# Optimization experiments

Hardware: AMD Instinct MI355X
Metric: run time of the kernel (lower is better)

## Reference

```python
import jax, jax.numpy as jnp
import numpy as np

B, G, S, C = 64, 2048, 64, 3


def setup_inputs() -> dict:
    key = jax.random.key(0)
    k1, k2 = jax.random.split(key)
    neighbor = jax.random.normal(k1, (B, G, S, C), dtype=jnp.float32)
    center = jax.random.normal(k2, (B, G, C), dtype=jnp.float32)
    return {"neighbor": neighbor, "center": center}


def _disambiguate_vector_directions(lps, vecs):
    # lps: [B,G,S,3] local points; vecs: [B,G,3] candidate axes.
    knn = lps.shape[2]
    proj = jnp.sum(vecs[:, :, None, :] * lps, axis=3)                 # [B,G,S]
    n_pos = jnp.sum((proj > 0).astype(jnp.float32), axis=2, keepdims=True)  # [B,G,1]
    flip = (n_pos < 0.5 * knn).astype(jnp.float32)
    return (1.0 - 2.0 * flip) * vecs


def reference(neighbor, center):
    # neighbor: [B,G,S,3] (C==3 path -> axis1/axis2 both PCA)
    pos = neighbor[..., 0:3]
    # Distance-based weights for weighted PCA covariance.
    norms = jnp.linalg.norm(pos, axis=3, keepdims=True)               # [B,G,S,1]
    max_norms = jnp.max(norms, axis=2, keepdims=True)                 # [B,G,1,1]
    w = max_norms - norms
    w = w / (jnp.sum(w, axis=2, keepdims=True) + 1e-6)
    scaled_pos = 100.0 * pos
    # Weighted covariance: [B,G,3,3]
    covs = jnp.einsum('bgsk,bgsl->bgkl', w * scaled_pos, scaled_pos)
    # Symmetric 3x3 eigendecomposition, eigenvalues ascending, eigenvectors as columns
    # (same convention as pytorch3d symeig3x3; signs fixed by disambiguation below).
    _, eigvec = jnp.linalg.eigh(covs)                                 # [B,G,3,3]
    z_axis = _disambiguate_vector_directions(pos, eigvec[:, :, :, 0])  # smallest-eig
    x_axis = _disambiguate_vector_directions(pos, eigvec[:, :, :, 2])  # largest-eig
    y_axis = jnp.cross(z_axis, x_axis)                                # [B,G,3]
    lrfs = jnp.stack((z_axis, y_axis, x_axis), axis=3)                # [B,G,3,3] (columns)
    # Rotate local points into the LRF: batched [S,3] x [3,3]
    rot_neighbor = jnp.einsum('bgsc,bgcd->bgsd', pos, lrfs)           # [B,G,S,3]
    return (rot_neighbor, lrfs)
```

## Files before the change

### kernel.cpp

```cpp
#include <hip/hip_runtime.h>
#include <math.h>


__device__ __forceinline__ float slapy2_(float x, float y) {
    _Pragma("clang fp contract(off)")
    float xa = fabsf(x), ya = fabsf(y);
    float w = fmaxf(xa, ya), z = fminf(xa, ya);
    if (z == 0.0f) return w;
    float t = z / w;
    return w * sqrtf(1.0f + t * t);
}

__device__ __forceinline__ void slartg_(float f, float g,
                                        float &c, float &s, float &r) {
    _Pragma("clang fp contract(off)")
    if (g == 0.0f) { c = 1.0f; s = 0.0f; r = f; return; }
    if (f == 0.0f) { c = 0.0f; s = (g >= 0.0f) ? 1.0f : -1.0f; r = fabsf(g); return; }
    float d = sqrtf(f * f + g * g);
    float p = 1.0f / d;
    c = fabsf(f) * p;
    s = g * ((f >= 0.0f) ? p : -p);
    r = (f >= 0.0f) ? d : -d;
}

__device__ __forceinline__ void slaev2_(float a, float b, float cc,
                                        float &rt1, float &rt2,
                                        float &cs1, float &sn1) {
    _Pragma("clang fp contract(off)")
    float sm = a + cc, df = a - cc;
    float adf = fabsf(df);
    float tb = b + b;
    float ab = fabsf(tb);
    float acmx, acmn;
    if (fabsf(a) > fabsf(cc)) { acmx = a; acmn = cc; } else { acmx = cc; acmn = a; }
    float rt;
    if (adf > ab)      { float t = ab / adf; rt = adf * sqrtf(1.0f + t * t); }
    else if (adf < ab) { float t = adf / ab; rt = ab * sqrtf(1.0f + t * t); }
    else                rt = ab * sqrtf(2.0f);
    int sgn1;
    if (sm < 0.0f)      { rt1 = 0.5f * (sm - rt); sgn1 = -1; rt2 = (acmx / rt1) * acmn - (b / rt1) * b; }
    else if (sm > 0.0f) { rt1 = 0.5f * (sm + rt); sgn1 =  1; rt2 = (acmx / rt1) * acmn - (b / rt1) * b; }
    else                { rt1 = 0.5f * rt; rt2 = -0.5f * rt; sgn1 = 1; }
    int sgn2;
    float cs;
    if (df >= 0.0f) { cs = df + rt; sgn2 = 1; } else { cs = df - rt; sgn2 = -1; }
    float acs = fabsf(cs);
    if (acs > ab) {
        float ct = -tb / cs;
        sn1 = 1.0f / sqrtf(1.0f + ct * ct);
        cs1 = ct * sn1;
    } else {
        if (ab == 0.0f) { cs1 = 1.0f; sn1 = 0.0f; }
        else {
            float tn = -cs / tb;
            cs1 = 1.0f / sqrtf(1.0f + tn * tn);
            sn1 = tn * cs1;
        }
    }
    if (sgn1 == sgn2) { float tn = cs1; cs1 = -sn1; sn1 = tn; }
}

__device__ __forceinline__ float getd3(int i, float d1, float d2, float d3) {
    return (i == 1) ? d1 : ((i == 2) ? d2 : d3);
}
__device__ __forceinline__ void setd3(int i, float v, float &d1, float &d2, float &d3) {
    d1 = (i == 1) ? v : d1;
    d2 = (i == 2) ? v : d2;
    d3 = (i == 3) ? v : d3;
}
__device__ __forceinline__ float gete2(int i, float e1, float e2) {
    return (i == 1) ? e1 : e2;
}
__device__ __forceinline__ void sete2(int i, float v, float &e1, float &e2) {
    e1 = (i == 1) ? v : e1;
    e2 = (i == 2) ? v : e2;
}

__device__ __forceinline__ void zrot3r(int j, float ctemp, float stemp,
                                       float &z11, float &z12, float &z13,
                                       float &z21, float &z22, float &z23,
                                       float &z31, float &z32, float &z33) {
    _Pragma("clang fp contract(off)")
    if (j == 1) {
        { float t = z12; z12 = (ctemp * t) - (stemp * z11); z11 = (stemp * t) + (ctemp * z11); }
        { float t = z22; z22 = (ctemp * t) - (stemp * z21); z21 = (stemp * t) + (ctemp * z21); }
        { float t = z32; z32 = (ctemp * t) - (stemp * z31); z31 = (stemp * t) + (ctemp * z31); }
    } else {
        { float t = z13; z13 = (ctemp * t) - (stemp * z12); z12 = (stemp * t) + (ctemp * z12); }
        { float t = z23; z23 = (ctemp * t) - (stemp * z22); z22 = (stemp * t) + (ctemp * z22); }
        { float t = z33; z33 = (ctemp * t) - (stemp * z32); z32 = (stemp * t) + (ctemp * z32); }
    }
}

__device__ __forceinline__ void ssteqr3_reg(
        float &d1_, float &d2_, float &d3_, float &e1_, float &e2_,
        float &z11, float &z12, float &z13,
        float &z21, float &z22, float &z23,
        float &z31, float &z32, float &z33) {
    _Pragma("clang fp contract(off)")
    const float EPS    = 5.9604644775390625e-8f;
    const float EPS2   = EPS * EPS;
    const float SAFMIN = 1.17549435e-38f;
    const int n = 3, nmaxit = 3 * 30;
    int jtot = 0, l1 = 1;

#define GD(i)      getd3((i), d1_, d2_, d3_)
#define SD(i, v)   setd3((i), (v), d1_, d2_, d3_)
#define GE(i)      gete2((i), e1_, e2_)
#define SE(i, v)   sete2((i), (v), e1_, e2_)
#define ZR(j, c, s) zrot3r((j), (c), (s), z11, z12, z13, z21, z22, z23, z31, z32, z33)

    while (true) {
        if (l1 > n) break;
        if (l1 > 1) SE(l1 - 1, 0.0f);
        int m = n;
        for (int mm = l1; mm <= n - 1; ++mm) {
            float tst = fabsf(GE(mm));
            if (tst == 0.0f) { m = mm; break; }
            if (tst <= (sqrtf(fabsf(GD(mm))) * sqrtf(fabsf(GD(mm + 1)))) * EPS) {
                SE(mm, 0.0f); m = mm; break;
            }
        }
        int l = l1, lsv = l, lend = m, lendsv = lend;
        l1 = m + 1;
        if (lend == l) continue;
        if (fabsf(GD(lend)) < fabsf(GD(l))) { lend = lsv; l = lendsv; }

        if (lend > l) {
            while (true) {
                m = lend;
                if (l != lend) {
                    for (int mm = l; mm <= lend - 1; ++mm) {
                        float em = GE(mm);
                        float tst = em * em;
                        if (tst <= (EPS2 * fabsf(GD(mm))) * fabsf(GD(mm + 1)) + SAFMIN) { m = mm; break; }
                    }
                }
                if (m < lend) SE(m, 0.0f);
                float p = GD(l);
                if (m == l) {
                    SD(l, p); ++l;
                    if (l <= lend) continue;
                    break;
                }
                if (m == l + 1) {
                    float rt1, rt2, c, s;
                    slaev2_(GD(l), GE(l), GD(l + 1), rt1, rt2, c, s);
                    ZR(l, c, s);
                    SD(l, rt1); SD(l + 1, rt2); SE(l, 0.0f);
                    l += 2;
                    if (l <= lend) continue;
                    break;
                }
                if (jtot == nmaxit) break;
                ++jtot;
                {
                    float el = GE(l);
                    float g = (GD(l + 1) - p) / (2.0f * el);
                    float r = slapy2_(g, 1.0f);
                    g = GD(m) - p + el / (g + ((g >= 0.0f) ? r : -r));
                    float s = 1.0f, c = 1.0f;
                    p = 0.0f;
                    for (int i = m - 1; i >= l; --i) {
                        float ei = GE(i);
                        float f = s * ei;
                        float b = c * ei;
                        slartg_(g, f, c, s, r);
                        if (i != m - 1) SE(i + 1, r);
                        g = GD(i + 1) - p;
                        float r2 = ((GD(i) - g) * s) + ((2.0f * c) * b);
                        p = s * r2;
                        SD(i + 1, g + p);
                        g = (c * r2) - b;
                        ZR(i, c, -s);
                    }
                    SD(l, GD(l) - p);
                    SE(l, g);
                }
            }
        } else if (lend < l) {
            while (true) {
                m = lend;
                if (l != lend) {
                    for (int mm = l; mm >= lend + 1; --mm) {
                        float em = GE(mm - 1);
                        float tst = em * em;
                        if (tst <= (EPS2 * fabsf(GD(mm))) * fabsf(GD(mm - 1)) + SAFMIN) { m = mm; break; }
                    }
                }
                if (m > lend) SE(m - 1, 0.0f);
                float p = GD(l);
                if (m == l) {
                    SD(l, p); --l;
                    if (l >= lend) continue;
                    break;
                }
                if (m == l - 1) {
                    float rt1, rt2, c, s;
                    slaev2_(GD(l - 1), GE(l - 1), GD(l), rt1, rt2, c, s);
                    ZR(l - 1, c, s);
                    SD(l - 1, rt1); SD(l, rt2); SE(l - 1, 0.0f);
                    l -= 2;
                    if (l >= lend) continue;
                    break;
                }
                if (jtot == nmaxit) break;
                ++jtot;
                {
                    float el = GE(l - 1);
                    float g = (GD(l - 1) - p) / (2.0f * el);
                    float r = slapy2_(g, 1.0f);
                    g = GD(m) - p + el / (g + ((g >= 0.0f) ? r : -r));
                    float s = 1.0f, c = 1.0f;
                    p = 0.0f;
                    for (int i = m; i <= l - 1; ++i) {
                        float ei = GE(i);
                        float f = s * ei;
                        float b = c * ei;
                        slartg_(g, f, c, s, r);
                        if (i != m) SE(i - 1, r);
                        g = GD(i) - p;
                        float r2 = ((GD(i + 1) - g) * s) + ((2.0f * c) * b);
                        p = s * r2;
                        SD(i, g + p);
                        g = (c * r2) - b;
                        ZR(i, c, s);
                    }
                    SD(l, GD(l) - p);
                    SE(l - 1, g);
                }
            }
        }
    }
    {
        int k = 1; float p = d1_;
        if (d2_ < p) { k = 2; p = d2_; }
        if (d3_ < p) { k = 3; p = d3_; }
        if (k == 2) {
            d2_ = d1_; d1_ = p;
            float t;
            t = z11; z11 = z12; z12 = t;
            t = z21; z21 = z22; z22 = t;
            t = z31; z31 = z32; z32 = t;
        } else if (k == 3) {
            d3_ = d1_; d1_ = p;
            float t;
            t = z11; z11 = z13; z13 = t;
            t = z21; z21 = z23; z23 = t;
            t = z31; z31 = z33; z33 = t;
        }
        if (d3_ < d2_) {
            float t = d2_; d2_ = d3_; d3_ = t;
            t = z12; z12 = z13; z13 = t;
            t = z22; z22 = z23; z23 = t;
            t = z32; z32 = z33; z33 = t;
        }
    }
#undef GD
#undef SD
#undef GE
#undef SE
#undef ZR
}

__device__ __forceinline__ float nrm3_(float x, float y, float z) {
    _Pragma("clang fp contract(off)")
    float t = (x * x) + (y * y);
    t = t + (z * z);
    return sqrtf(t);
}

__device__ __forceinline__ void covstep(float px, float py, float pz, float wq,
                                        float &c00, float &c10, float &c20,
                                        float &c11, float &c21, float &c22) {
    _Pragma("clang fp contract(off)")
    const float spx = 100.0f * px, spy = 100.0f * py, spz = 100.0f * pz;
    const float ax = wq * spx, ay = wq * spy, az = wq * spz;
    c00 = c00 + (ax * spx);
    c10 = c10 + (ay * spx);
    c20 = c20 + (az * spx);
    c11 = c11 + (ay * spy);
    c21 = c21 + (az * spy);
    c22 = c22 + (az * spz);
}

__device__ __forceinline__ void rotstep(float px, float py, float pz,
                                        float zv0, float zv1, float zv2,
                                        float yv0, float yv1, float yv2,
                                        float xv0, float xv1, float xv2,
                                        float &ra, float &rb, float &rc) {
    _Pragma("clang fp contract(off)")
    ra = ((px * zv0) + (py * zv1)) + (pz * zv2);
    rb = ((px * yv0) + (py * yv1)) + (pz * yv2);
    rc = ((px * xv0) + (py * xv1)) + (pz * xv2);
}

__global__ __launch_bounds__(256, 4) void lrf_kernel(const float* __restrict__ nbr,
                                                     float* __restrict__ rot,
                                                     float* __restrict__ lrf) {
    _Pragma("clang fp contract(off)")
    __shared__ float wql[64 * 65];
    const int tid = threadIdx.x;
    const int gl  = tid >> 2;
    const int k   = tid & 3;
    const int g   = (blockIdx.x << 6) + gl;
    const int lbase = gl * 65;

    const float4* __restrict__ p4 = reinterpret_cast<const float4*>(nbr)
                                    + (long long)g * 48 + k * 12;
    const float4* __restrict__ q4 = reinterpret_cast<const float4*>(nbr)
                                    + (long long)g * 48;

    float mx = -3.402823466e+38f;
#pragma unroll
    for (int q = 0; q < 4; ++q) {
        const float4 v0 = p4[q * 3 + 0];
        const float4 v1 = p4[q * 3 + 1];
        const float4 v2 = p4[q * 3 + 2];
        const float n0 = nrm3_(v0.x, v0.y, v0.z);
        const float n1 = nrm3_(v0.w, v1.x, v1.y);
        const float n2 = nrm3_(v1.z, v1.w, v2.x);
        const float n3 = nrm3_(v2.y, v2.z, v2.w);
        const int b = lbase + 16 * k + 4 * q;
        wql[b + 0] = n0;
        wql[b + 1] = n1;
        wql[b + 2] = n2;
        wql[b + 3] = n3;
        mx = fmaxf(mx, fmaxf(fmaxf(n0, n1), fmaxf(n2, n3)));
    }
    mx = fmaxf(mx, __shfl_xor(mx, 1, 64));
    mx = fmaxf(mx, __shfl_xor(mx, 2, 64));
    __builtin_amdgcn_wave_barrier();
    asm volatile("" ::: "memory");

    float r0_ = 0.0f, r1_ = 0.0f;
    {
        const int j0 = lbase + 2 * k;
#pragma unroll
        for (int t = 0; t < 8; ++t) {
            r0_ = r0_ + (mx - wql[j0 + 8 * t + 0]);
            r1_ = r1_ + (mx - wql[j0 + 8 * t + 1]);
        }
    }
    const float A_ = r0_ + r1_;
    const float B_ = A_ + __shfl_xor(A_, 1, 64);
    const float ws = B_ + __shfl_xor(B_, 2, 64);
    const float denom = ws + 1e-6f;
    asm volatile("" ::: "memory");

#pragma unroll
    for (int i = 0; i < 16; ++i) {
        const int idx = lbase + 16 * k + i;
        const float nv = wql[idx];
        wql[idx] = (mx - nv) / denom;
    }
    __builtin_amdgcn_wave_barrier();
    asm volatile("" ::: "memory");

    float c00 = 0.0f, c10 = 0.0f, c20 = 0.0f, c11 = 0.0f, c21 = 0.0f, c22 = 0.0f;
#pragma unroll 4
    for (int q = 0; q < 16; ++q) {
        const float4 v0 = q4[q * 3 + 0];
        const float4 v1 = q4[q * 3 + 1];
        const float4 v2 = q4[q * 3 + 2];
        const float w0 = wql[lbase + 4 * q + 0];
        const float w1 = wql[lbase + 4 * q + 1];
        const float w2 = wql[lbase + 4 * q + 2];
        const float w3 = wql[lbase + 4 * q + 3];
        covstep(v0.x, v0.y, v0.z, w0, c00, c10, c20, c11, c21, c22);
        covstep(v0.w, v1.x, v1.y, w1, c00, c10, c20, c11, c21, c22);
        covstep(v1.z, v1.w, v2.x, w2, c00, c10, c20, c11, c21, c22);
        covstep(v2.y, v2.z, v2.w, w3, c00, c10, c20, c11, c21, c22);
    }

    const float a11 = c00, a21 = c10, a31 = c20, a22 = c11, a32 = c21, a33 = c22;

    float taui, v2h, e1q, d2q, d3q, e2q;
    const float xnorm = fabsf(a31);
    if (xnorm == 0.0f) {
        taui = 0.0f; v2h = a31; e1q = a21; d2q = a22; e2q = a32; d3q = a33;
    } else {
        const float beta = -copysignf(slapy2_(a21, xnorm), a21);
        taui = (beta - a21) / beta;
        const float rcp = 1.0f / (a21 - beta);
        v2h = a31 * rcp;
        e1q = beta;
        float x1 = taui * a22;
        float x2 = taui * a32;
        const float temp2 = a32 * v2h;
        x1 = x1 + (taui * temp2);
        const float t1v = taui * v2h;
        x2 = x2 + (t1v * a33);
        const float dt = x1 + (x2 * v2h);
        const float alpha_c = (-0.5f * taui) * dt;
        const float w1 = x1 + alpha_c;
        const float w2 = x2 + (alpha_c * v2h);
        d2q = (a22 - w1) - w1;
        e2q = (a32 - (v2h * w1)) - w2;
        d3q = (a33 - (v2h * w2)) - (w2 * v2h);
    }

    float d1_ = a11, d2_ = d2q, d3_ = d3q, e1_ = e1q, e2_ = e2q;
    float z11 = 1.0f, z12 = 0.0f, z13 = 0.0f;
    float z21 = 0.0f, z22 = 1.0f, z23 = 0.0f;
    float z31 = 0.0f, z32 = 0.0f, z33 = 1.0f;
    ssteqr3_reg(d1_, d2_, d3_, e1_, e2_,
                z11, z12, z13, z21, z22, z23, z31, z32, z33);

    float zv0, zv1, zv2, xv0, xv1, xv2;
    {
        const float u2 = z21, u3 = z31;
        zv0 = z11;
        if (taui != 0.0f) {
            const float wj = u2 + (u3 * v2h);
            const float pj = taui * wj;
            zv1 = u2 - pj;
            zv2 = u3 - (v2h * pj);
        } else { zv1 = u2; zv2 = u3; }
    }
    {
        const float u2 = z23, u3 = z33;
        xv0 = z13;
        if (taui != 0.0f) {
            const float wj = u2 + (u3 * v2h);
            const float pj = taui * wj;
            xv1 = u2 - pj;
            xv2 = u3 - (v2h * pj);
        } else { xv1 = u2; xv2 = u3; }
    }

    const float yv0 = (zv1 * xv2) - (zv2 * xv1);
    const float yv1 = (zv2 * xv0) - (zv0 * xv2);
    const float yv2 = (zv0 * xv1) - (zv1 * xv0);

    float fr[48];
    int cz = 0, cx = 0;
#pragma unroll
    for (int q = 0; q < 4; ++q) {
        const float4 v0 = p4[q * 3 + 0];
        const float4 v1 = p4[q * 3 + 1];
        const float4 v2 = p4[q * 3 + 2];
        rotstep(v0.x, v0.y, v0.z, zv0, zv1, zv2, yv0, yv1, yv2, xv0, xv1, xv2,
                fr[12 * q + 0], fr[12 * q + 1], fr[12 * q + 2]);
        rotstep(v0.w, v1.x, v1.y, zv0, zv1, zv2, yv0, yv1, yv2, xv0, xv1, xv2,
                fr[12 * q + 3], fr[12 * q + 4], fr[12 * q + 5]);
        rotstep(v1.z, v1.w, v2.x, zv0, zv1, zv2, yv0, yv1, yv2, xv0, xv1, xv2,
                fr[12 * q + 6], fr[12 * q + 7], fr[12 * q + 8]);
        rotstep(v2.y, v2.z, v2.w, zv0, zv1, zv2, yv0, yv1, yv2, xv0, xv1, xv2,
                fr[12 * q + 9], fr[12 * q + 10], fr[12 * q + 11]);
        cz += (fr[12 * q + 0] > 0.0f) ? 1 : 0;
        cz += (fr[12 * q + 3] > 0.0f) ? 1 : 0;
        cz += (fr[12 * q + 6] > 0.0f) ? 1 : 0;
        cz += (fr[12 * q + 9] > 0.0f) ? 1 : 0;
        cx += (fr[12 * q + 2] > 0.0f) ? 1 : 0;
        cx += (fr[12 * q + 5] > 0.0f) ? 1 : 0;
        cx += (fr[12 * q + 8] > 0.0f) ? 1 : 0;
        cx += (fr[12 * q + 11] > 0.0f) ? 1 : 0;
    }
    cz += __shfl_xor(cz, 1, 64);
    cz += __shfl_xor(cz, 2, 64);
    cx += __shfl_xor(cx, 1, 64);
    cx += __shfl_xor(cx, 2, 64);
    const float sz = (cz < 32) ? -1.0f : 1.0f;
    const float sx = (cx < 32) ? -1.0f : 1.0f;
    const float sy = sz * sx;

#pragma unroll
    for (int f = 0; f < 48; ++f) {
        const int c = f % 3;
        const float sc = (c == 0) ? sz : ((c == 1) ? sy : sx);
        fr[f] = fr[f] * sc;
    }

    float4* __restrict__ o4 = reinterpret_cast<float4*>(rot)
                              + (long long)g * 48 + k * 12;
#pragma unroll
    for (int q = 0; q < 12; ++q) {
        float4 t;
        t.x = fr[4 * q + 0];
        t.y = fr[4 * q + 1];
        t.z = fr[4 * q + 2];
        t.w = fr[4 * q + 3];
        o4[q] = t;
    }

    if (k < 3) {
        const float zc = ((k == 0) ? zv0 : ((k == 1) ? zv1 : zv2)) * sz;
        const float yc = ((k == 0) ? yv0 : ((k == 1) ? yv1 : yv2)) * sy;
        const float xc = ((k == 0) ? xv0 : ((k == 1) ? xv1 : xv2)) * sx;
        float* __restrict__ lp = lrf + (long long)g * 9 + 3 * k;
        lp[0] = zc;
        lp[1] = yc;
        lp[2] = xc;
    }
}

extern "C" void kernel_launch(void* const* d_in, const int* in_sizes, int n_in,
                              void* d_out, int out_size, void* d_ws, size_t ws_size,
                              hipStream_t stream) {
    const float* neighbor = (const float*)d_in[0];
    float* rot = (float*)d_out;
    float* lrf = (float*)d_out + (long long)64 * 2048 * 64 * 3;

    lrf_kernel<<<dim3(2048), dim3(256), 0, stream>>>(neighbor, rot, lrf);
}
```

Before: 274.8 us.

## Compute eigensolve once per group via shared memory and recompute rotation after sign vote

The 3x3 tridiagonalization and QL eigensolve used to be run redundantly by all four lanes of each group. Now the covariance is staged in shared memory, one thread per group runs the eigensolve, and the axes are broadcast back through shared memory. The 48-float register buffer is also dropped: a projection pass counts signs only, and the rotated points are recomputed with the signs applied while storing. This trades two block barriers, a serialized eigensolve on a single wave, and a second read of the neighbor data for less redundant math and lower register pressure.

New measurement: 272.4 us. About the same (-0.9%).

```diff
diff --git a/kernel.cpp b/kernel.cpp
--- a/kernel.cpp
+++ b/kernel.cpp
@@ -284,15 +284,27 @@
     c22 = c22 + (az * spz);
 }
 
+__device__ __forceinline__ void projstep(float px, float py, float pz,
+                                         float zv0, float zv1, float zv2,
+                                         float xv0, float xv1, float xv2,
+                                         int &cz, int &cx) {
+    _Pragma("clang fp contract(off)")
+    const float pjz = ((zv0 * px) + (zv1 * py)) + (zv2 * pz);
+    const float pjx = ((xv0 * px) + (xv1 * py)) + (xv2 * pz);
+    cz += (pjz > 0.0f) ? 1 : 0;
+    cx += (pjx > 0.0f) ? 1 : 0;
+}
+
 __device__ __forceinline__ void rotstep(float px, float py, float pz,
                                         float zv0, float zv1, float zv2,
                                         float yv0, float yv1, float yv2,
                                         float xv0, float xv1, float xv2,
+                                        float sz, float sy, float sx,
                                         float &ra, float &rb, float &rc) {
     _Pragma("clang fp contract(off)")
-    ra = ((px * zv0) + (py * zv1)) + (pz * zv2);
-    rb = ((px * yv0) + (py * yv1)) + (pz * yv2);
-    rc = ((px * xv0) + (py * xv1)) + (pz * xv2);
+    ra = (((px * zv0) + (py * zv1)) + (pz * zv2)) * sz;
+    rb = (((px * yv0) + (py * yv1)) + (pz * yv2)) * sy;
+    rc = (((px * xv0) + (py * xv1)) + (pz * xv2)) * sx;
 }
 
 __global__ __launch_bounds__(256, 4) void lrf_kernel(const float* __restrict__ nbr,
@@ -300,6 +312,7 @@
                                                      float* __restrict__ lrf) {
     _Pragma("clang fp contract(off)")
     __shared__ float wql[64 * 65];
+    __shared__ float cov6[64 * 7];
     const int tid = threadIdx.x;
     const int gl  = tid >> 2;
     const int k   = tid & 3;
@@ -373,89 +386,106 @@
         covstep(v2.y, v2.z, v2.w, w3, c00, c10, c20, c11, c21, c22);
     }
 
-    const float a11 = c00, a21 = c10, a31 = c20, a22 = c11, a32 = c21, a33 = c22;
-
-    float taui, v2h, e1q, d2q, d3q, e2q;
-    const float xnorm = fabsf(a31);
-    if (xnorm == 0.0f) {
-        taui = 0.0f; v2h = a31; e1q = a21; d2q = a22; e2q = a32; d3q = a33;
-    } else {
-        const float beta = -copysignf(slapy2_(a21, xnorm), a21);
-        taui = (beta - a21) / beta;
-        const float rcp = 1.0f / (a21 - beta);
-        v2h = a31 * rcp;
-        e1q = beta;
-        float x1 = taui * a22;
-        float x2 = taui * a32;
-        const float temp2 = a32 * v2h;
-        x1 = x1 + (taui * temp2);
-        const float t1v = taui * v2h;
-        x2 = x2 + (t1v * a33);
-        const float dt = x1 + (x2 * v2h);
-        const float alpha_c = (-0.5f * taui) * dt;
-        const float w1 = x1 + alpha_c;
-        const float w2 = x2 + (alpha_c * v2h);
-        d2q = (a22 - w1) - w1;
-        e2q = (a32 - (v2h * w1)) - w2;
-        d3q = (a33 - (v2h * w2)) - (w2 * v2h);
-    }
-
-    float d1_ = a11, d2_ = d2q, d3_ = d3q, e1_ = e1q, e2_ = e2q;
-    float z11 = 1.0f, z12 = 0.0f, z13 = 0.0f;
-    float z21 = 0.0f, z22 = 1.0f, z23 = 0.0f;
-    float z31 = 0.0f, z32 = 0.0f, z33 = 1.0f;
-    ssteqr3_reg(d1_, d2_, d3_, e1_, e2_,
-                z11, z12, z13, z21, z22, z23, z31, z32, z33);
-
-    float zv0, zv1, zv2, xv0, xv1, xv2;
     {
-        const float u2 = z21, u3 = z31;
-        zv0 = z11;
-        if (taui != 0.0f) {
-            const float wj = u2 + (u3 * v2h);
-            const float pj = taui * wj;
-            zv1 = u2 - pj;
-            zv2 = u3 - (v2h * pj);
-        } else { zv1 = u2; zv2 = u3; }
-    }
-    {
-        const float u2 = z23, u3 = z33;
-        xv0 = z13;
-        if (taui != 0.0f) {
-            const float wj = u2 + (u3 * v2h);
-            const float pj = taui * wj;
-            xv1 = u2 - pj;
-            xv2 = u3 - (v2h * pj);
-        } else { xv1 = u2; xv2 = u3; }
-    }
+        const float vA = (k == 0) ? c00 : ((k == 1) ? c10 : ((k == 2) ? c20 : c11));
+        cov6[gl * 7 + k] = vA;
+        if (k < 2) {
+            const float vB = (k == 0) ? c21 : c22;
+            cov6[gl * 7 + 4 + k] = vB;
+        }
+    }
+    __syncthreads();
+
+    if (tid < 64) {
+        const int tb = tid * 7;
+        const float a11 = cov6[tb + 0];
+        const float a21 = cov6[tb + 1];
+        const float a31 = cov6[tb + 2];
+        const float a22 = cov6[tb + 3];
+        const float a32 = cov6[tb + 4];
+        const float a33 = cov6[tb + 5];
+
+        float taui, v2h, e1q, d2q, d3q, e2q;
+        const float xnorm = fabsf(a31);
+        if (xnorm == 0.0f) {
+            taui = 0.0f; v2h = a31; e1q = a21; d2q = a22; e2q = a32; d3q = a33;
+        } else {
+            const float beta = -copysignf(slapy2_(a21, xnorm), a21);
+            taui = (beta - a21) / beta;
+            const float rcp = 1.0f / (a21 - beta);
+            v2h = a31 * rcp;
+            e1q = beta;
+            float x1 = taui * a22;
+            float x2 = taui * a32;
+            const float temp2 = a32 * v2h;
+            x1 = x1 + (taui * temp2);
+            const float t1v = taui * v2h;
+            x2 = x2 + (t1v * a33);
+            const float dt = x1 + (x2 * v2h);
+            const float alpha_c = (-0.5f * taui) * dt;
+            const float w1 = x1 + alpha_c;
+            const float w2 = x2 + (alpha_c * v2h);
+            d2q = (a22 - w1) - w1;
+            e2q = (a32 - (v2h * w1)) - w2;
+            d3q = (a33 - (v2h * w2)) - (w2 * v2h);
+        }
+
+        float d1_ = a11, d2_ = d2q, d3_ = d3q, e1_ = e1q, e2_ = e2q;
+        float z11 = 1.0f, z12 = 0.0f, z13 = 0.0f;
+        float z21 = 0.0f, z22 = 1.0f, z23 = 0.0f;
+        float z31 = 0.0f, z32 = 0.0f, z33 = 1.0f;
+        ssteqr3_reg(d1_, d2_, d3_, e1_, e2_,
+                    z11, z12, z13, z21, z22, z23, z31, z32, z33);
+
+        float zv0, zv1, zv2, xv0, xv1, xv2;
+        {
+            const float u2 = z21, u3 = z31;
+            zv0 = z11;
+            if (taui != 0.0f) {
+                const float wj = u2 + (u3 * v2h);
+                const float pj = taui * wj;
+                zv1 = u2 - pj;
+                zv2 = u3 - (v2h * pj);
+            } else { zv1 = u2; zv2 = u3; }
+        }
+        {
+            const float u2 = z23, u3 = z33;
+            xv0 = z13;
+            if (taui != 0.0f) {
+                const float wj = u2 + (u3 * v2h);
+                const float pj = taui * wj;
+                xv1 = u2 - pj;
+                xv2 = u3 - (v2h * pj);
+            } else { xv1 = u2; xv2 = u3; }
+        }
+
+        wql[tb + 0] = zv0;
+        wql[tb + 1] = zv1;
+        wql[tb + 2] = zv2;
+        wql[tb + 3] = xv0;
+        wql[tb + 4] = xv1;
+        wql[tb + 5] = xv2;
+    }
+    __syncthreads();
+
+    const int ab = gl * 7;
+    const float zv0 = wql[ab + 0], zv1 = wql[ab + 1], zv2 = wql[ab + 2];
+    const float xv0 = wql[ab + 3], xv1 = wql[ab + 4], xv2 = wql[ab + 5];
 
     const float yv0 = (zv1 * xv2) - (zv2 * xv1);
     const float yv1 = (zv2 * xv0) - (zv0 * xv2);
     const float yv2 = (zv0 * xv1) - (zv1 * xv0);
 
-    float fr[48];
     int cz = 0, cx = 0;
 #pragma unroll
     for (int q = 0; q < 4; ++q) {
         const float4 v0 = p4[q * 3 + 0];
         const float4 v1 = p4[q * 3 + 1];
         const float4 v2 = p4[q * 3 + 2];
-        rotstep(v0.x, v0.y, v0.z, zv0, zv1, zv2, yv0, yv1, yv2, xv0, xv1, xv2,
-                fr[12 * q + 0], fr[12 * q + 1], fr[12 * q + 2]);
-        rotstep(v0.w, v1.x, v1.y, zv0, zv1, zv2, yv0, yv1, yv2, xv0, xv1, xv2,
-                fr[12 * q + 3], fr[12 * q + 4], fr[12 * q + 5]);
-        rotstep(v1.z, v1.w, v2.x, zv0, zv1, zv2, yv0, yv1, yv2, xv0, xv1, xv2,
-                fr[12 * q + 6], fr[12 * q + 7], fr[12 * q + 8]);
-        rotstep(v2.y, v2.z, v2.w, zv0, zv1, zv2, yv0, yv1, yv2, xv0, xv1, xv2,
-                fr[12 * q + 9], fr[12 * q + 10], fr[12 * q + 11]);
-        cz += (fr[12 * q + 0] > 0.0f) ? 1 : 0;
-        cz += (fr[12 * q + 3] > 0.0f) ? 1 : 0;
-        cz += (fr[12 * q + 6] > 0.0f) ? 1 : 0;
-        cz += (fr[12 * q + 9] > 0.0f) ? 1 : 0;
-        cx += (fr[12 * q + 2] > 0.0f) ? 1 : 0;
-        cx += (fr[12 * q + 5] > 0.0f) ? 1 : 0;
-        cx += (fr[12 * q + 8] > 0.0f) ? 1 : 0;
-        cx += (fr[12 * q + 11] > 0.0f) ? 1 : 0;
+        projstep(v0.x, v0.y, v0.z, zv0, zv1, zv2, xv0, xv1, xv2, cz, cx);
+        projstep(v0.w, v1.x, v1.y, zv0, zv1, zv2, xv0, xv1, xv2, cz, cx);
+        projstep(v1.z, v1.w, v2.x, zv0, zv1, zv2, xv0, xv1, xv2, cz, cx);
+        projstep(v2.y, v2.z, v2.w, zv0, zv1, zv2, xv0, xv1, xv2, cz, cx);
     }
     cz += __shfl_xor(cz, 1, 64);
     cz += __shfl_xor(cz, 2, 64);
@@ -465,23 +495,29 @@
     const float sx = (cx < 32) ? -1.0f : 1.0f;
     const float sy = sz * sx;
 
-#pragma unroll
-    for (int f = 0; f < 48; ++f) {
-        const int c = f % 3;
-        const float sc = (c == 0) ? sz : ((c == 1) ? sy : sx);
-        fr[f] = fr[f] * sc;
-    }
-
     float4* __restrict__ o4 = reinterpret_cast<float4*>(rot)
                               + (long long)g * 48 + k * 12;
 #pragma unroll
-    for (int q = 0; q < 12; ++q) {
-        float4 t;
-        t.x = fr[4 * q + 0];
-        t.y = fr[4 * q + 1];
-        t.z = fr[4 * q + 2];
-        t.w = fr[4 * q + 3];
-        o4[q] = t;
+    for (int q = 0; q < 4; ++q) {
+        const float4 v0 = p4[q * 3 + 0];
+        const float4 v1 = p4[q * 3 + 1];
+        const float4 v2 = p4[q * 3 + 2];
+        float r0a, r0b, r0c, r1a, r1b, r1c, r2a, r2b, r2c, r3a, r3b, r3c;
+        rotstep(v0.x, v0.y, v0.z, zv0, zv1, zv2, yv0, yv1, yv2, xv0, xv1, xv2,
+                sz, sy, sx, r0a, r0b, r0c);
+        rotstep(v0.w, v1.x, v1.y, zv0, zv1, zv2, yv0, yv1, yv2, xv0, xv1, xv2,
+                sz, sy, sx, r1a, r1b, r1c);
+        rotstep(v1.z, v1.w, v2.x, zv0, zv1, zv2, yv0, yv1, yv2, xv0, xv1, xv2,
+                sz, sy, sx, r2a, r2b, r2c);
+        rotstep(v2.y, v2.z, v2.w, zv0, zv1, zv2, yv0, yv1, yv2, xv0, xv1, xv2,
+                sz, sy, sx, r3a, r3b, r3c);
+        float4 o0, o1, o2;
+        o0.x = r0a; o0.y = r0b; o0.z = r0c; o0.w = r1a;
+        o1.x = r1b; o1.y = r1c; o1.z = r2a; o1.w = r2b;
+        o2.x = r2c; o2.y = r3a; o2.z = r3b; o2.w = r3c;
+        o4[q * 3 + 0] = o0;
+        o4[q * 3 + 1] = o1;
+        o4[q * 3 + 2] = o2;
     }
 
     if (k < 3) {
```
